# Kernel optimization log

Hardware: AMD Instinct MI355X
Metric: run time of the kernel (lower is better)

Reference implementation:

```python
import jax, jax.numpy as jnp
import numpy as np

B, S, E = 8, 2048, 768
N, H = 12, 64
INIT = 0.02
IGNORE = -100000.0


def setup_inputs() -> dict:
    key = jax.random.key(0)
    ks = jax.random.split(key, 5)
    return {
        "normalized_resid_pre": jax.random.normal(ks[0], (B, S, E), jnp.float32),
        "W_Q": jax.random.normal(ks[1], (N, E, H), jnp.float32) * INIT,
        "W_K": jax.random.normal(ks[2], (N, E, H), jnp.float32) * INIT,
        "W_V": jax.random.normal(ks[3], (N, E, H), jnp.float32) * INIT,
        "W_O": jax.random.normal(ks[4], (N, H, E), jnp.float32) * INIT,
        "b_Q": jnp.zeros((N, H), jnp.float32),
        "b_K": jnp.zeros((N, H), jnp.float32),
        "b_V": jnp.zeros((N, H), jnp.float32),
        "b_O": jnp.zeros((E,), jnp.float32),
    }


def reference(normalized_resid_pre, W_Q, W_K, W_V, W_O, b_Q, b_K, b_V, b_O):
    x = normalized_resid_pre
    b, s, e = x.shape
    d_head = W_Q.shape[-1]
    q = jnp.einsum('bse,neh->bsnh', x, W_Q) + b_Q  # [b, sq, n, h]
    k = jnp.einsum('bse,neh->bsnh', x, W_K) + b_K
    v = jnp.einsum('bse,neh->bsnh', x, W_V) + b_V
    scores = jnp.einsum('bqnh,bknh->bnqk', q, k) / jnp.sqrt(jnp.float32(d_head))
    mask = jnp.tril(jnp.ones((s, s), jnp.float32))  # [sq, sk]
    masked = mask * scores + (1.0 - mask) * IGNORE
    probs = jax.nn.softmax(masked, axis=-1)
    z = jnp.einsum('bnqk,bknh->bqnh', probs, v)
    # sum over heads of per-head output projection + bias
    out = jnp.einsum('bqnh,nhe->bqe', z, W_O) + b_O
    return out
```

## Files before the change

### kernel.cpp

```cpp
#include <hip/hip_runtime.h>
#include <hip/hip_bf16.h>
#include <stdint.h>


#define B_ 8
#define S_ 2048
#define E_ 768
#define NHEADS 12
#define HD 64
#define BS (B_*S_)
#define NHD (NHEADS*HD)

typedef short bf16x8 __attribute__((ext_vector_type(8)));
typedef short bf16x4 __attribute__((ext_vector_type(4)));
typedef float f32x4  __attribute__((ext_vector_type(4)));
typedef __hip_bfloat16 bf16;

typedef const __attribute__((address_space(1))) char* as1_t;
typedef __attribute__((address_space(3))) char* as3_t;

__device__ __forceinline__ f32x4 mfma16(bf16x8 a, bf16x8 b, f32x4 c) {
    return __builtin_amdgcn_mfma_f32_16x16x32_bf16(a, b, c, 0, 0, 0);
}
__device__ __forceinline__ bf16x8 ld8(const bf16* p) {
    return *reinterpret_cast<const bf16x8*>(p);
}
__device__ __forceinline__ void gload16(const bf16* g, bf16* l) {
    __builtin_amdgcn_global_load_lds((as1_t)g, (as3_t)l, 16, 0, 0);
}
__device__ __forceinline__ bf16x8 pack8(f32x4 a, f32x4 b) {
    union { bf16x8 v; __hip_bfloat162 h[4]; } u;
    u.h[0] = __float22bfloat162_rn(make_float2(a[0], a[1]));
    u.h[1] = __float22bfloat162_rn(make_float2(a[2], a[3]));
    u.h[2] = __float22bfloat162_rn(make_float2(b[0], b[1]));
    u.h[3] = __float22bfloat162_rn(make_float2(b[2], b[3]));
    return u.v;
}

__global__ __launch_bounds__(256) void prep_kernel(
    const float* __restrict__ x,  const float* __restrict__ Wq,
    const float* __restrict__ Wk, const float* __restrict__ Wv,
    const float* __restrict__ Wo,
    bf16* __restrict__ xb,  bf16* __restrict__ WqT, bf16* __restrict__ WkT,
    bf16* __restrict__ WvT, bf16* __restrict__ WoT)
{
    const int tid = blockIdx.x * 256 + threadIdx.x;
    const int nth = gridDim.x * 256;
    for (int i = tid; i < BS*E_; i += nth)
        xb[i] = __float2bfloat16(x[i]);
    for (int i = tid; i < NHD*E_; i += nth) {
        const int c = i / E_;
        const int e = i - c*E_;
        const int n = c >> 6, h = c & 63;
        const int src = (n*E_ + e)*HD + h;
        WqT[i] = __float2bfloat16(Wq[src]);
        WkT[i] = __float2bfloat16(Wk[src]);
        WvT[i] = __float2bfloat16(Wv[src]);
        WoT[e*NHD + c] = __float2bfloat16(Wo[i]);
    }
}

#define STAGE_TILE(dst, src_base, lda, j, ks)                                   \
    gload16((src_base) + (size_t)((j)*16 + rowlo)*(lda) + (size_t)(ks)*32 + kc8,\
            &(dst)[(j)*512])

__global__ __launch_bounds__(256) void qkv_gemm(
    const bf16* __restrict__ xb,
    const bf16* __restrict__ WqT, const bf16* __restrict__ WkT, const bf16* __restrict__ WvT,
    const float* __restrict__ bq, const float* __restrict__ bk, const float* __restrict__ bv,
    bf16* __restrict__ Qb, bf16* __restrict__ Kb, bf16* __restrict__ VTb)
{
    __shared__ __align__(16) bf16 sA[2][4096];
    __shared__ __align__(16) bf16 sB[2][4096];

    const int tm  = blockIdx.x;
    const int tn  = blockIdx.y;
    const int mat = tn / 6;
    const int c0  = (tn - mat*6) * 128;
    const bf16* BT = (mat==0) ? WqT : (mat==1) ? WkT : WvT;
    const int lane = threadIdx.x & 63;
    const int w    = threadIdx.x >> 6;
    const int l16 = lane & 15, quad = lane >> 4;
    const int rowlo = lane & 15, kc8 = (lane >> 4)*8;
    const int r0  = tm*128 + (w>>1)*64;
    const int cc0 = c0 + (w&1)*64;
    const bf16* Abase = xb + (size_t)tm*128*E_;
    const bf16* Bbase = BT + (size_t)c0*E_;
    const int j0 = 2*w, j1 = 2*w + 1;
    const int rgA = (w>>1)*4, rgB = (w&1)*4;

    f32x4 acc[4][4];
    #pragma unroll
    for (int mt=0;mt<4;mt++)
        #pragma unroll
        for (int nt=0;nt<4;nt++) acc[mt][nt] = (f32x4){0.f,0.f,0.f,0.f};

    STAGE_TILE(sA[0], Abase, E_, j0, 0); STAGE_TILE(sA[0], Abase, E_, j1, 0);
    STAGE_TILE(sB[0], Bbase, E_, j0, 0); STAGE_TILE(sB[0], Bbase, E_, j1, 0);
    __syncthreads();

    const int KS = E_/32;
    int buf = 0;
    for (int ks = 0; ks < KS; ++ks) {
        if (ks + 1 < KS) {
            const int nb = buf ^ 1;
            STAGE_TILE(sA[nb], Abase, E_, j0, ks+1); STAGE_TILE(sA[nb], Abase, E_, j1, ks+1);
            STAGE_TILE(sB[nb], Bbase, E_, j0, ks+1); STAGE_TILE(sB[nb], Bbase, E_, j1, ks+1);
        }
        bf16x8 a[4], b[4];
        #pragma unroll
        for (int mt=0;mt<4;mt++) a[mt] = ld8(&sA[buf][(rgA+mt)*512 + lane*8]);
        #pragma unroll
        for (int nt=0;nt<4;nt++) b[nt] = ld8(&sB[buf][(rgB+nt)*512 + lane*8]);
        #pragma unroll
        for (int mt=0;mt<4;mt++)
            #pragma unroll
            for (int nt=0;nt<4;nt++)
                acc[mt][nt] = mfma16(a[mt], b[nt], acc[mt][nt]);
        __syncthreads();
        buf ^= 1;
    }

    const float* bias  = (mat==0) ? bq : (mat==1) ? bk : bv;
    const float  scale = (mat==0) ? 0.125f * 1.44269504088896340736f : 1.0f;
    bf16* dstQK = (mat==0) ? Qb : Kb;
    #pragma unroll
    for (int nt=0;nt<4;nt++) {
        const int col = cc0 + nt*16 + l16;
        const int hn = col >> 6, h = col & 63;
        const float bb = bias[col];
        #pragma unroll
        for (int mt=0;mt<4;mt++) {
            const int row = r0 + mt*16 + quad*4;
            const int bi = row >> 11;
            const int s  = row & (S_-1);
            if (mat < 2) {
                bf16* d = dstQK + ((size_t)(bi*NHEADS + hn)*S_ + s)*HD + h;
                #pragma unroll
                for (int r=0;r<4;r++)
                    d[(size_t)r*HD] = __float2bfloat16((acc[mt][nt][r] + bb)*scale);
            } else {
                bf16* d = VTb + ((size_t)(bi*NHEADS + hn)*HD + h)*S_ + s;
                #pragma unroll
                for (int r=0;r<4;r++)
                    d[r] = __float2bfloat16(acc[mt][nt][r] + bb);
            }
        }
    }
}

__global__ __launch_bounds__(256, 3) void attn_kernel(
    const bf16* __restrict__ Qb, const bf16* __restrict__ Kb,
    const bf16* __restrict__ VTb, bf16* __restrict__ Z)
{
    __shared__ __align__(16) bf16 sK[2][64*64];
    __shared__ __align__(16) bf16 sV[2][64*64];

    const int id = blockIdx.x;
    const int bx = id / 96;
    const int g  = id - bx*96;
    const int hn = g % NHEADS, b = g / NHEADS;
    const int tid  = threadIdx.x;
    const int w    = tid >> 6;
    const int lane = tid & 63;
    const int l16 = lane & 15, quad = lane >> 4;
    const size_t bn = (size_t)b*NHEADS + hn;

    const bf16* Qbase = Qb  + bn*S_*HD;
    const bf16* Kbase = Kb  + bn*S_*HD;
    const bf16* Vbase = VTb + bn*HD*S_;

    const int mA = tid, mB = tid + 256;
    const int rA = mA >> 3, cgA = mA & 7;
    const int rB = mB >> 3, cgB = mB & 7;
    const int slA = (rA*8 + ((cgA + rA + (rA>>3)) & 7)) * 8;
    const int slB = (rB*8 + ((cgB + rB + (rB>>3)) & 7)) * 8;
    const size_t vofA = (size_t)rA*S_ + cgA*8;
    const size_t vofB = (size_t)rB*S_ + cgB*8;

    const int kperm = (l16 >> 2)*8 + (l16 & 3);
    int kidx[2][2][2];
    #pragma unroll
    for (int c=0;c<2;c++)
        #pragma unroll
        for (int bg=0;bg<2;bg++)
            #pragma unroll
            for (int hf=0;hf<2;hf++) {
                const int r = 32*c + 4*bg + kperm;
                const int q = hf*4 + quad;
                kidx[c][bg][hf] = (r*8 + ((q + r + (r>>3)) & 7)) * 8;
            }
    int vidx[4][2];
    #pragma unroll
    for (int ht=0;ht<4;ht++)
        #pragma unroll
        for (int c=0;c<2;c++) {
            const int rho = ht*16 + l16;
            const int q = c*4 + quad;
            vidx[ht][c] = (rho*8 + ((q + rho + (rho>>3)) & 7)) * 8;
        }

    #pragma unroll
    for (int half = 0; half < 2; ++half) {
        const int qblk = half ? (S_/128 - 1 - bx) : bx;
        const int ktb  = 2*qblk + 1;
        const int ktw  = 2*qblk + (w >> 1);
        const int qbase = qblk*128 + w*32;

        bf16x8 bqf[2][2];
        #pragma unroll
        for (int qi=0;qi<2;qi++)
            #pragma unroll
            for (int hf=0;hf<2;hf++)
                bqf[qi][hf] = ld8(Qbase + (size_t)(qbase + qi*16 + l16)*HD + hf*32 + quad*8);

        f32x4 acc[2][4];
        #pragma unroll
        for (int qi=0;qi<2;qi++)
            #pragma unroll
            for (int ht=0;ht<4;ht++) acc[qi][ht] = (f32x4){0.f,0.f,0.f,0.f};
        float lsum[2] = {0.f, 0.f};

        bf16x8 k0 = ld8(Kbase + (size_t)mA*8);
        bf16x8 k1 = ld8(Kbase + (size_t)mB*8);
        bf16x8 v0 = ld8(Vbase + vofA);
        bf16x8 v1 = ld8(Vbase + vofB);
        *reinterpret_cast<bf16x8*>(&sK[0][slA]) = k0;
        *reinterpret_cast<bf16x8*>(&sK[0][slB]) = k1;
        *reinterpret_cast<bf16x8*>(&sV[0][slA]) = v0;
        *reinterpret_cast<bf16x8*>(&sV[0][slB]) = v1;
        __syncthreads();

        for (int kt = 0; kt <= ktb; ++kt) {
            if (kt < ktb) {
                const size_t kt1 = (size_t)(kt+1)*64;
                k0 = ld8(Kbase + kt1*HD + (size_t)mA*8);
                k1 = ld8(Kbase + kt1*HD + (size_t)mB*8);
                v0 = ld8(Vbase + vofA + kt1);
                v1 = ld8(Vbase + vofB + kt1);
            }
            if (kt <= ktw) {
                const bf16* kb = sK[kt & 1];
                const bf16* vb = sV[kt & 1];
                #pragma unroll
                for (int c=0;c<2;c++) {
                    const bf16x8 akA0 = ld8(kb + kidx[c][0][0]);
                    const bf16x8 akA1 = ld8(kb + kidx[c][0][1]);
                    const bf16x8 akB0 = ld8(kb + kidx[c][1][0]);
                    const bf16x8 akB1 = ld8(kb + kidx[c][1][1]);
                    bf16x8 av[4];
                    #pragma unroll
                    for (int ht=0;ht<4;ht++) av[ht] = ld8(vb + vidx[ht][c]);

                    #pragma unroll
                    for (int qi=0;qi<2;qi++) {
                        f32x4 s0 = (f32x4){0.f,0.f,0.f,0.f};
                        s0 = mfma16(akA0, bqf[qi][0], s0);
                        s0 = mfma16(akA1, bqf[qi][1], s0);
                        f32x4 s1 = (f32x4){0.f,0.f,0.f,0.f};
                        s1 = mfma16(akB0, bqf[qi][0], s1);
                        s1 = mfma16(akB1, bqf[qi][1], s1);
                        if (kt == ktw) {
                            const int q  = qbase + qi*16 + l16;
                            const int kb0 = kt*64 + c*32 + quad*8;
                            #pragma unroll
                            for (int r=0;r<4;r++) {
                                s0[r] = (kb0 + r     > q) ? -1e30f : s0[r];
                                s1[r] = (kb0 + 4 + r > q) ? -1e30f : s1[r];
                            }
                        }
                        float ls = 0.f;
                        #pragma unroll
                        for (int r=0;r<4;r++) {
                            s0[r] = __builtin_amdgcn_exp2f(s0[r]);
                            s1[r] = __builtin_amdgcn_exp2f(s1[r]);
                            ls += s0[r] + s1[r];
                        }
                        lsum[qi] += ls;
                        const bf16x8 pf = pack8(s0, s1);
                        #pragma unroll
                        for (int ht=0;ht<4;ht++)
                            acc[qi][ht] = mfma16(av[ht], pf, acc[qi][ht]);
                    }
                }
            }
            if (kt < ktb) {
                const int nb = (kt+1) & 1;
                *reinterpret_cast<bf16x8*>(&sK[nb][slA]) = k0;
                *reinterpret_cast<bf16x8*>(&sK[nb][slB]) = k1;
                *reinterpret_cast<bf16x8*>(&sV[nb][slA]) = v0;
                *reinterpret_cast<bf16x8*>(&sV[nb][slB]) = v1;
            }
            __syncthreads();
        }

        #pragma unroll
        for (int qi=0;qi<2;qi++) {
            float rs = lsum[qi];
            rs += __shfl_xor(rs, 16, 64);
            rs += __shfl_xor(rs, 32, 64);
            const float inv_l = 1.0f / rs;
            const int q = qbase + qi*16 + l16;
            bf16* zp = Z + ((size_t)b*S_ + q)*NHD + (size_t)hn*HD + quad*4;
            #pragma unroll
            for (int ht=0;ht<4;ht++) {
                union { bf16x4 v; bf16 e[4]; } u;
                #pragma unroll
                for (int r=0;r<4;r++) u.e[r] = __float2bfloat16(acc[qi][ht][r] * inv_l);
                *reinterpret_cast<bf16x4*>(zp + ht*16) = u.v;
            }
        }
    }
}

__global__ __launch_bounds__(256) void out_gemm(
    const bf16* __restrict__ Z, const bf16* __restrict__ WoT,
    const float* __restrict__ bo, float* __restrict__ out)
{
    __shared__ __align__(16) bf16 sA[2][4096];
    __shared__ __align__(16) bf16 sB[2][4096];

    const int tm = blockIdx.x, tn = blockIdx.y;
    const int lane = threadIdx.x & 63;
    const int w    = threadIdx.x >> 6;
    const int l16 = lane & 15, quad = lane >> 4;
    const int rowlo = lane & 15, kc8 = (lane >> 4)*8;
    const int r0  = tm*128 + (w>>1)*64;
    const int cc0 = tn*128 + (w&1)*64;
    const bf16* Abase = Z   + (size_t)tm*128*NHD;
    const bf16* Bbase = WoT + (size_t)tn*128*NHD;
    const int j0 = 2*w, j1 = 2*w + 1;
    const int rgA = (w>>1)*4, rgB = (w&1)*4;

    f32x4 acc[4][4];
    #pragma unroll
    for (int mt=0;mt<4;mt++)
        #pragma unroll
        for (int nt=0;nt<4;nt++) acc[mt][nt] = (f32x4){0.f,0.f,0.f,0.f};

    STAGE_TILE(sA[0], Abase, NHD, j0, 0); STAGE_TILE(sA[0], Abase, NHD, j1, 0);
    STAGE_TILE(sB[0], Bbase, NHD, j0, 0); STAGE_TILE(sB[0], Bbase, NHD, j1, 0);
    __syncthreads();

    const int KS = NHD/32;
    int buf = 0;
    for (int ks = 0; ks < KS; ++ks) {
        if (ks + 1 < KS) {
            const int nb = buf ^ 1;
            STAGE_TILE(sA[nb], Abase, NHD, j0, ks+1); STAGE_TILE(sA[nb], Abase, NHD, j1, ks+1);
            STAGE_TILE(sB[nb], Bbase, NHD, j0, ks+1); STAGE_TILE(sB[nb], Bbase, NHD, j1, ks+1);
        }
        bf16x8 a[4], b[4];
        #pragma unroll
        for (int mt=0;mt<4;mt++) a[mt] = ld8(&sA[buf][(rgA+mt)*512 + lane*8]);
        #pragma unroll
        for (int nt=0;nt<4;nt++) b[nt] = ld8(&sB[buf][(rgB+nt)*512 + lane*8]);
        #pragma unroll
        for (int mt=0;mt<4;mt++)
            #pragma unroll
            for (int nt=0;nt<4;nt++)
                acc[mt][nt] = mfma16(a[mt], b[nt], acc[mt][nt]);
        __syncthreads();
        buf ^= 1;
    }

    #pragma unroll
    for (int nt=0;nt<4;nt++) {
        const int col = cc0 + nt*16 + l16;
        const float bb = bo[col];
        #pragma unroll
        for (int mt=0;mt<4;mt++) {
            float* d = out + (size_t)(r0 + mt*16 + quad*4)*E_ + col;
            #pragma unroll
            for (int r=0;r<4;r++)
                d[(size_t)r*E_] = acc[mt][nt][r] + bb;
        }
    }
}

extern "C" void kernel_launch(void* const* d_in, const int* in_sizes, int n_in,
                              void* d_out, int out_size, void* d_ws, size_t ws_size,
                              hipStream_t stream)
{
    const float* x  = (const float*)d_in[0];
    const float* Wq = (const float*)d_in[1];
    const float* Wk = (const float*)d_in[2];
    const float* Wv = (const float*)d_in[3];
    const float* Wo = (const float*)d_in[4];
    const float* bq = (const float*)d_in[5];
    const float* bk = (const float*)d_in[6];
    const float* bv = (const float*)d_in[7];
    const float* bo = (const float*)d_in[8];
    float* out = (float*)d_out;

    char* ws = (char*)d_ws;
    size_t off = 0;
    auto alloc = [&](size_t bytes){ char* p = ws + off; off += (bytes + 255) & ~(size_t)255; return p; };
    bf16* xb  = (bf16*)alloc((size_t)BS*E_*2);
    bf16* WqT = (bf16*)alloc((size_t)NHD*E_*2);
    bf16* WkT = (bf16*)alloc((size_t)NHD*E_*2);
    bf16* WvT = (bf16*)alloc((size_t)NHD*E_*2);
    bf16* WoT = (bf16*)alloc((size_t)E_*NHD*2);
    bf16* Qb  = (bf16*)alloc((size_t)BS*NHD*2);
    bf16* Kb  = (bf16*)alloc((size_t)BS*NHD*2);
    bf16* VTb = (bf16*)alloc((size_t)BS*NHD*2);
    bf16* Zb  = (bf16*)alloc((size_t)BS*NHD*2);

    prep_kernel<<<4096, 256, 0, stream>>>(x, Wq, Wk, Wv, Wo, xb, WqT, WkT, WvT, WoT);
    qkv_gemm<<<dim3(BS/128, 18), 256, 0, stream>>>(xb, WqT, WkT, WvT, bq, bk, bv, Qb, Kb, VTb);
    attn_kernel<<<768, 256, 0, stream>>>(Qb, Kb, VTb, Zb);
    out_gemm<<<dim3(BS/128, E_/128), 256, 0, stream>>>(Zb, WoT, bo, out);
}
```

Measured before the change: 258.8 us.

## Rewrite QKV and output GEMMs as 256x256 tiled, 8-wave pipelined kernels

Replaces the 128x128 tile QKV and output-projection GEMMs with 256x256 tiles computed by 512-thread blocks. K is staged in 64-wide slabs, and a hand-scheduled phase loop interleaves global-to-LDS loads with MFMAs, using explicit barriers, vmcnt waits and s_setprio. The QKV weights are packed into one contiguous buffer so a single kernel covers all three projections, and V^T stores become 4-wide vector writes. The goal is more operand reuse per LDS load and better hiding of memory latency. In exchange the kernels use much more LDS and registers and launch fewer blocks: the output GEMM gets only 192 blocks.

```diff
diff --git a/kernel.cpp b/kernel.cpp
--- a/kernel.cpp
+++ b/kernel.cpp
@@ -60,91 +60,145 @@
     }
 }
 
-#define STAGE_TILE(dst, src_base, lda, j, ks)                                   \
-    gload16((src_base) + (size_t)((j)*16 + rowlo)*(lda) + (size_t)(ks)*32 + kc8,\
-            &(dst)[(j)*512])
-
-__global__ __launch_bounds__(256) void qkv_gemm(
-    const bf16* __restrict__ xb,
-    const bf16* __restrict__ WqT, const bf16* __restrict__ WkT, const bf16* __restrict__ WvT,
+
+#define FENCE() asm volatile("" ::: "memory")
+#define VMCNT4() asm volatile("s_waitcnt vmcnt(4)" ::: "memory")
+
+#define STG(dst, gbase, kt, rh) do {                                              \
+    const bf16* _s = (gbase) + (size_t)((rh)*128 + w*16 + l16)*768 + (kt)*64 + kc8;\
+    gload16(_s,      &(dst)[((rh)*2 + 0)*4096 + w*512]);                          \
+    gload16(_s + 32, &(dst)[((rh)*2 + 1)*4096 + w*512]);                          \
+} while (0)
+
+#define PHASE(bufA, bufB, q, LOADB, STAGE, WAIT) do {                             \
+    if (LOADB) {                                                                  \
+        _Pragma("unroll") for (int n = 0; n < 4; ++n)                             \
+        _Pragma("unroll") for (int ks = 0; ks < 2; ++ks)                          \
+            bfr[n][ks] = ld8(&(bufB)[((wn>>1)*2 + ks)*4096 +                      \
+                                     ((wn&1)*4 + n)*512 + lane*8]);               \
+    }                                                                             \
+    bf16x8 afr[2][2];                                                             \
+    _Pragma("unroll") for (int m = 0; m < 2; ++m)                                 \
+    _Pragma("unroll") for (int ks = 0; ks < 2; ++ks)                              \
+        afr[m][ks] = ld8(&(bufA)[(wm*2 + ks)*4096 + ((q)*2 + m)*512 + lane*8]);   \
+    STAGE;                                                                        \
+    FENCE(); __builtin_amdgcn_s_barrier(); FENCE();                               \
+    asm volatile("s_waitcnt lgkmcnt(0)" ::: "memory");                            \
+    __builtin_amdgcn_s_setprio(1);                                                \
+    _Pragma("unroll") for (int m = 0; m < 2; ++m)                                 \
+    _Pragma("unroll") for (int n = 0; n < 4; ++n)                                 \
+    _Pragma("unroll") for (int ks = 0; ks < 2; ++ks)                              \
+        acc[(q)*2 + m][n] = mfma16(afr[m][ks], bfr[n][ks], acc[(q)*2 + m][n]);    \
+    __builtin_amdgcn_s_setprio(0);                                                \
+    WAIT;                                                                         \
+    FENCE(); __builtin_amdgcn_s_barrier(); FENCE();                               \
+} while (0)
+
+#define GEMM256_BODY(Ab, Bb)                                                      \
+    f32x4 acc[8][4];                                                              \
+    _Pragma("unroll") for (int mf = 0; mf < 8; ++mf)                              \
+    _Pragma("unroll") for (int nf = 0; nf < 4; ++nf)                              \
+        acc[mf][nf] = (f32x4){0.f, 0.f, 0.f, 0.f};                                \
+    bf16x8 bfr[4][2];                                                             \
+    STG(sA[0], Ab, 0, 0); STG(sA[0], Ab, 0, 1);                                   \
+    STG(sB[0], Bb, 0, 0); STG(sB[0], Bb, 0, 1);                                   \
+    STG(sB[1], Bb, 1, 0); STG(sB[1], Bb, 1, 1);                                   \
+    VMCNT4();                                                                     \
+    FENCE(); __builtin_amdgcn_s_barrier(); FENCE();                               \
+    _Pragma("unroll 1")                                                           \
+    for (int i = 0; i < 6; ++i) {                                                 \
+        const int kA  = 2*i + 1;                                                  \
+        const int kN  = (2*i + 2 < 12) ? 2*i + 2 : 11;                            \
+        const int kN3 = (2*i + 3 < 12) ? 2*i + 3 : 11;                            \
+        PHASE(sA[0], sB[0], 0, 1, STG(sA[1], Ab, kA,  0), (void)0);               \
+        PHASE(sA[0], sB[0], 1, 0, STG(sA[1], Ab, kA,  1), (void)0);               \
+        PHASE(sA[0], sB[0], 2, 0, STG(sB[0], Bb, kN,  0), (void)0);               \
+        PHASE(sA[0], sB[0], 3, 0, STG(sB[0], Bb, kN,  1), VMCNT4());              \
+        PHASE(sA[1], sB[1], 0, 1, STG(sA[0], Ab, kN,  0), (void)0);               \
+        PHASE(sA[1], sB[1], 1, 0, STG(sA[0], Ab, kN,  1), (void)0);               \
+        PHASE(sA[1], sB[1], 2, 0, STG(sB[1], Bb, kN3, 0), (void)0);               \
+        PHASE(sA[1], sB[1], 3, 0, STG(sB[1], Bb, kN3, 1), VMCNT4());              \
+    }
+
+__global__ __launch_bounds__(512, 2) void qkv_gemm256(
+    const bf16* __restrict__ xb, const bf16* __restrict__ WT,
     const float* __restrict__ bq, const float* __restrict__ bk, const float* __restrict__ bv,
     bf16* __restrict__ Qb, bf16* __restrict__ Kb, bf16* __restrict__ VTb)
 {
-    __shared__ __align__(16) bf16 sA[2][4096];
-    __shared__ __align__(16) bf16 sB[2][4096];
-
-    const int tm  = blockIdx.x;
-    const int tn  = blockIdx.y;
-    const int mat = tn / 6;
-    const int c0  = (tn - mat*6) * 128;
-    const bf16* BT = (mat==0) ? WqT : (mat==1) ? WkT : WvT;
+    __shared__ __align__(16) bf16 sA[2][16384];
+    __shared__ __align__(16) bf16 sB[2][16384];
+
+    const int tm = blockIdx.x, tn = blockIdx.y;
     const int lane = threadIdx.x & 63;
     const int w    = threadIdx.x >> 6;
+    const int wm = w >> 2, wn = w & 3;
     const int l16 = lane & 15, quad = lane >> 4;
-    const int rowlo = lane & 15, kc8 = (lane >> 4)*8;
-    const int r0  = tm*128 + (w>>1)*64;
-    const int cc0 = c0 + (w&1)*64;
-    const bf16* Abase = xb + (size_t)tm*128*E_;
-    const bf16* Bbase = BT + (size_t)c0*E_;
-    const int j0 = 2*w, j1 = 2*w + 1;
-    const int rgA = (w>>1)*4, rgB = (w&1)*4;
-
-    f32x4 acc[4][4];
-    #pragma unroll
-    for (int mt=0;mt<4;mt++)
-        #pragma unroll
-        for (int nt=0;nt<4;nt++) acc[mt][nt] = (f32x4){0.f,0.f,0.f,0.f};
-
-    STAGE_TILE(sA[0], Abase, E_, j0, 0); STAGE_TILE(sA[0], Abase, E_, j1, 0);
-    STAGE_TILE(sB[0], Bbase, E_, j0, 0); STAGE_TILE(sB[0], Bbase, E_, j1, 0);
-    __syncthreads();
-
-    const int KS = E_/32;
-    int buf = 0;
-    for (int ks = 0; ks < KS; ++ks) {
-        if (ks + 1 < KS) {
-            const int nb = buf ^ 1;
-            STAGE_TILE(sA[nb], Abase, E_, j0, ks+1); STAGE_TILE(sA[nb], Abase, E_, j1, ks+1);
-            STAGE_TILE(sB[nb], Bbase, E_, j0, ks+1); STAGE_TILE(sB[nb], Bbase, E_, j1, ks+1);
-        }
-        bf16x8 a[4], b[4];
-        #pragma unroll
-        for (int mt=0;mt<4;mt++) a[mt] = ld8(&sA[buf][(rgA+mt)*512 + lane*8]);
-        #pragma unroll
-        for (int nt=0;nt<4;nt++) b[nt] = ld8(&sB[buf][(rgB+nt)*512 + lane*8]);
-        #pragma unroll
-        for (int mt=0;mt<4;mt++)
-            #pragma unroll
-            for (int nt=0;nt<4;nt++)
-                acc[mt][nt] = mfma16(a[mt], b[nt], acc[mt][nt]);
-        __syncthreads();
-        buf ^= 1;
-    }
-
-    const float* bias  = (mat==0) ? bq : (mat==1) ? bk : bv;
-    const float  scale = (mat==0) ? 0.125f * 1.44269504088896340736f : 1.0f;
+    const int kc8 = quad * 8;
+    const bf16* Ab = xb + (size_t)tm*256*E_;
+    const bf16* Bb = WT + (size_t)tn*256*E_;
+
+    GEMM256_BODY(Ab, Bb);
+
+    const int mat = tn / 3;
+    const int cloc0 = (tn - mat*3)*256 + wn*64;
+    const float* bias = (mat==0) ? bq : (mat==1) ? bk : bv;
+    const float scale = (mat==0) ? 0.125f * 1.44269504088896340736f : 1.0f;
     bf16* dstQK = (mat==0) ? Qb : Kb;
     #pragma unroll
-    for (int nt=0;nt<4;nt++) {
-        const int col = cc0 + nt*16 + l16;
+    for (int nf = 0; nf < 4; ++nf) {
+        const int col = cloc0 + nf*16 + l16;
         const int hn = col >> 6, h = col & 63;
         const float bb = bias[col];
         #pragma unroll
-        for (int mt=0;mt<4;mt++) {
-            const int row = r0 + mt*16 + quad*4;
+        for (int mf = 0; mf < 8; ++mf) {
+            const int row = tm*256 + wm*128 + mf*16 + quad*4;
             const int bi = row >> 11;
             const int s  = row & (S_-1);
             if (mat < 2) {
                 bf16* d = dstQK + ((size_t)(bi*NHEADS + hn)*S_ + s)*HD + h;
                 #pragma unroll
-                for (int r=0;r<4;r++)
-                    d[(size_t)r*HD] = __float2bfloat16((acc[mt][nt][r] + bb)*scale);
+                for (int r = 0; r < 4; ++r)
+                    d[(size_t)r*HD] = __float2bfloat16((acc[mf][nf][r] + bb)*scale);
             } else {
                 bf16* d = VTb + ((size_t)(bi*NHEADS + hn)*HD + h)*S_ + s;
+                union { bf16x4 v; bf16 e[4]; } u;
                 #pragma unroll
-                for (int r=0;r<4;r++)
-                    d[r] = __float2bfloat16(acc[mt][nt][r] + bb);
-            }
+                for (int r = 0; r < 4; ++r) u.e[r] = __float2bfloat16(acc[mf][nf][r] + bb);
+                *reinterpret_cast<bf16x4*>(d) = u.v;
+            }
+        }
+    }
+}
+
+__global__ __launch_bounds__(512, 2) void out_gemm256(
+    const bf16* __restrict__ Z, const bf16* __restrict__ WoT,
+    const float* __restrict__ bo, float* __restrict__ out)
+{
+    __shared__ __align__(16) bf16 sA[2][16384];
+    __shared__ __align__(16) bf16 sB[2][16384];
+
+    const int tm = blockIdx.x, tn = blockIdx.y;
+    const int lane = threadIdx.x & 63;
+    const int w    = threadIdx.x >> 6;
+    const int wm = w >> 2, wn = w & 3;
+    const int l16 = lane & 15, quad = lane >> 4;
+    const int kc8 = quad * 8;
+    const bf16* Ab = Z   + (size_t)tm*256*NHD;
+    const bf16* Bb = WoT + (size_t)tn*256*NHD;
+
+    GEMM256_BODY(Ab, Bb);
+
+    #pragma unroll
+    for (int nf = 0; nf < 4; ++nf) {
+        const int col = tn*256 + wn*64 + nf*16 + l16;
+        const float bb = bo[col];
+        #pragma unroll
+        for (int mf = 0; mf < 8; ++mf) {
+            const int row = tm*256 + wm*128 + mf*16 + quad*4;
+            float* d = out + (size_t)row*E_ + col;
+            #pragma unroll
+            for (int r = 0; r < 4; ++r)
+                d[(size_t)r*E_] = acc[mf][nf][r] + bb;
         }
     }
 }
@@ -313,71 +367,6 @@
     }
 }
 
-__global__ __launch_bounds__(256) void out_gemm(
-    const bf16* __restrict__ Z, const bf16* __restrict__ WoT,
-    const float* __restrict__ bo, float* __restrict__ out)
-{
-    __shared__ __align__(16) bf16 sA[2][4096];
-    __shared__ __align__(16) bf16 sB[2][4096];
-
-    const int tm = blockIdx.x, tn = blockIdx.y;
-    const int lane = threadIdx.x & 63;
-    const int w    = threadIdx.x >> 6;
-    const int l16 = lane & 15, quad = lane >> 4;
-    const int rowlo = lane & 15, kc8 = (lane >> 4)*8;
-    const int r0  = tm*128 + (w>>1)*64;
-    const int cc0 = tn*128 + (w&1)*64;
-    const bf16* Abase = Z   + (size_t)tm*128*NHD;
-    const bf16* Bbase = WoT + (size_t)tn*128*NHD;
-    const int j0 = 2*w, j1 = 2*w + 1;
-    const int rgA = (w>>1)*4, rgB = (w&1)*4;
-
-    f32x4 acc[4][4];
-    #pragma unroll
-    for (int mt=0;mt<4;mt++)
-        #pragma unroll
-        for (int nt=0;nt<4;nt++) acc[mt][nt] = (f32x4){0.f,0.f,0.f,0.f};
-
-    STAGE_TILE(sA[0], Abase, NHD, j0, 0); STAGE_TILE(sA[0], Abase, NHD, j1, 0);
-    STAGE_TILE(sB[0], Bbase, NHD, j0, 0); STAGE_TILE(sB[0], Bbase, NHD, j1, 0);
-    __syncthreads();
-
-    const int KS = NHD/32;
-    int buf = 0;
-    for (int ks = 0; ks < KS; ++ks) {
-        if (ks + 1 < KS) {
-            const int nb = buf ^ 1;
-            STAGE_TILE(sA[nb], Abase, NHD, j0, ks+1); STAGE_TILE(sA[nb], Abase, NHD, j1, ks+1);
-            STAGE_TILE(sB[nb], Bbase, NHD, j0, ks+1); STAGE_TILE(sB[nb], Bbase, NHD, j1, ks+1);
-        }
-        bf16x8 a[4], b[4];
-        #pragma unroll
-        for (int mt=0;mt<4;mt++) a[mt] = ld8(&sA[buf][(rgA+mt)*512 + lane*8]);
-        #pragma unroll
-        for (int nt=0;nt<4;nt++) b[nt] = ld8(&sB[buf][(rgB+nt)*512 + lane*8]);
-        #pragma unroll
-        for (int mt=0;mt<4;mt++)
-            #pragma unroll
-            for (int nt=0;nt<4;nt++)
-                acc[mt][nt] = mfma16(a[mt], b[nt], acc[mt][nt]);
-        __syncthreads();
-        buf ^= 1;
-    }
-
-    #pragma unroll
-    for (int nt=0;nt<4;nt++) {
-        const int col = cc0 + nt*16 + l16;
-        const float bb = bo[col];
-        #pragma unroll
-        for (int mt=0;mt<4;mt++) {
-            float* d = out + (size_t)(r0 + mt*16 + quad*4)*E_ + col;
-            #pragma unroll
-            for (int r=0;r<4;r++)
-                d[(size_t)r*E_] = acc[mt][nt][r] + bb;
-        }
-    }
-}
-
 extern "C" void kernel_launch(void* const* d_in, const int* in_sizes, int n_in,
                               void* d_out, int out_size, void* d_ws, size_t ws_size,
                               hipStream_t stream)
@@ -397,17 +386,19 @@
     size_t off = 0;
     auto alloc = [&](size_t bytes){ char* p = ws + off; off += (bytes + 255) & ~(size_t)255; return p; };
     bf16* xb  = (bf16*)alloc((size_t)BS*E_*2);
-    bf16* WqT = (bf16*)alloc((size_t)NHD*E_*2);
-    bf16* WkT = (bf16*)alloc((size_t)NHD*E_*2);
-    bf16* WvT = (bf16*)alloc((size_t)NHD*E_*2);
+    bf16* WT  = (bf16*)alloc((size_t)3*NHD*E_*2);
     bf16* WoT = (bf16*)alloc((size_t)E_*NHD*2);
     bf16* Qb  = (bf16*)alloc((size_t)BS*NHD*2);
     bf16* Kb  = (bf16*)alloc((size_t)BS*NHD*2);
     bf16* VTb = (bf16*)alloc((size_t)BS*NHD*2);
     bf16* Zb  = (bf16*)alloc((size_t)BS*NHD*2);
 
+    bf16* WqT = WT;
+    bf16* WkT = WT + (size_t)NHD*E_;
+    bf16* WvT = WT + (size_t)2*NHD*E_;
+
     prep_kernel<<<4096, 256, 0, stream>>>(x, Wq, Wk, Wv, Wo, xb, WqT, WkT, WvT, WoT);
-    qkv_gemm<<<dim3(BS/128, 18), 256, 0, stream>>>(xb, WqT, WkT, WvT, bq, bk, bv, Qb, Kb, VTb);
+    qkv_gemm256<<<dim3(BS/256, 9), 512, 0, stream>>>(xb, WT, bq, bk, bv, Qb, Kb, VTb);
     attn_kernel<<<768, 256, 0, stream>>>(Qb, Kb, VTb, Zb);
-    out_gemm<<<dim3(BS/128, E_/128), 256, 0, stream>>>(Zb, WoT, bo, out);
-}
+    out_gemm256<<<dim3(BS/256, E_/256), 512, 0, stream>>>(Zb, WoT, bo, out);
+}
```

After: 249.2 us. -3.7%, faster.
